# Optimization experiments

Hardware: AMD Instinct MI355X
Metric: run time of the kernel (lower is better)

Reference implementation:

```python
import jax, jax.numpy as jnp
import numpy as np

B, E, D, H, A = 65536, 16, 256, 64, 18  # batch, n_subpolicies, emb_dim, hidden, n_actions


def setup_inputs() -> dict:
    key = jax.random.key(0)
    ks = jax.random.split(key, 16)
    s = lambda k, sh: jax.random.normal(k, sh, dtype=jnp.float32) * 0.05
    return dict(
        obs=s(ks[0], (B, D)),
        h=s(ks[1], (B, D)),
        c=s(ks[2], (B, D)),
        idxs=jax.random.randint(ks[3], (B,), 0, E, dtype=jnp.int32),
        # Observer: LSTMCell(D, D) params (torch layout: [4D, D] with i,f,g,o gate order)
        W_ih=s(ks[4], (4 * D, D)), W_hh=s(ks[5], (4 * D, D)),
        b_ih=s(ks[6], (4 * D,)), b_hh=s(ks[7], (4 * D,)),
        # Stacked SubPolicy actor params: Linear(D,64)-Tanh-Linear(64,A)
        Wa1=s(ks[8], (E, D, H)), ba1=s(ks[9], (E, H)),
        Wa2=s(ks[10], (E, H, A)), ba2=s(ks[11], (E, A)),
        # Stacked SubPolicy critic params: Linear(D,64)-Tanh-Linear(64,1)
        Wc1=s(ks[12], (E, D, H)), bc1=s(ks[13], (E, H)),
        Wc2=s(ks[14], (E, H, 1)), bc2=s(ks[15], (E, 1)),
    )


def reference(obs, h, c, idxs, W_ih, W_hh, b_ih, b_hh,
              Wa1, ba1, Wa2, ba2, Wc1, bc1, Wc2, bc2):
    # ---- Observer: single LSTMCell step ----
    gates = obs @ W_ih.T + b_ih + h @ W_hh.T + b_hh          # [B, 4D]
    gi, gf, gg, go = jnp.split(gates, 4, axis=1)
    i = jax.nn.sigmoid(gi); f = jax.nn.sigmoid(gf); o = jax.nn.sigmoid(go)
    c_new = f * c + i * jnp.tanh(gg)                          # [B, D]
    h_new = o * jnp.tanh(c_new)                               # [B, D]

    # ---- Expert dispatch: evaluate all tiny subpolicy MLPs, select per sample ----
    # (mathematically identical to the per-sample routing loop in forward_sub)
    ha = jnp.tanh(jnp.einsum('bd,edh->beh', h_new, Wa1) + ba1)        # [B, E, H]
    logits_all = jnp.einsum('beh,eha->bea', ha, Wa2) + ba2            # [B, E, A]
    hc = jnp.tanh(jnp.einsum('bd,edh->beh', h_new, Wc1) + bc1)        # [B, E, H]
    vals_all = (jnp.einsum('beh,eho->beo', hc, Wc2) + bc2)[..., 0]    # [B, E]

    b = jnp.arange(h_new.shape[0])
    logits = logits_all[b, idxs]                                       # [B, A]
    values = vals_all[b, idxs]                                         # [B]
    return (h_new, c_new, logits, values)
```

## Files before the change

### kernel.cpp

```cpp
#include <hip/hip_runtime.h>
#include <hip/hip_bf16.h>
#include <math.h>

#define NB 65536
#define ND 256
#define NE 16
#define NH 64
#define NA 18

typedef __bf16 bf16;
typedef __bf16 bf16x4 __attribute__((ext_vector_type(4)));
typedef __bf16 bf16x8 __attribute__((ext_vector_type(8)));
typedef float  f32x4  __attribute__((ext_vector_type(4)));

#define OFF_WCAT 0u
#define OFF_BCAT 1048576u
#define OFF_PW1  1052672u
#define OFF_B1   2101248u
#define OFF_CUR  2109440u
#define OFF_PERM 2109504u

__device__ __forceinline__ float rcp_(float x) { return __builtin_amdgcn_rcpf(x); }
__device__ __forceinline__ float sigm_(float x) { return rcp_(1.f + __expf(-x)); }
__device__ __forceinline__ float tanh_(float x) {
    float cl = fminf(fmaxf(x, -15.f), 15.f);
    float e = __expf(2.f * cl);
    return (e - 1.f) * rcp_(e + 1.f);
}

__device__ __forceinline__ void gl2lds16(const void* g, void* l) {
    __builtin_amdgcn_global_load_lds(
        (const __attribute__((address_space(1))) unsigned int*)g,
        (__attribute__((address_space(3))) unsigned int*)l, 16, 0, 0);
}

__global__ void k_prep1(const float* __restrict__ W_ih, const float* __restrict__ W_hh,
                        const float* __restrict__ b_ih, const float* __restrict__ b_hh,
                        char* __restrict__ ws) {
    int t = blockIdx.x * 256 + threadIdx.x;
    int kstep = t >> 13;
    int cb    = (t >> 11) & 3;
    int idx   = t & 2047;
    int kf = idx >> 10, g = (idx >> 8) & 3, lk = (idx >> 6) & 3, u = idx & 63;
    int col = g * 256 + cb * 64 + (u ^ lk);
    int k0  = kstep * 64 + (kf * 4 + lk) * 8;
    const float* src = (k0 < 256) ? (W_ih + (size_t)col * 256 + k0)
                                  : (W_hh + (size_t)col * 256 + (k0 - 256));
    float4 v0 = *(const float4*)(src);
    float4 v1 = *(const float4*)(src + 4);
    bf16x8 o;
    o[0] = (bf16)v0.x; o[1] = (bf16)v0.y; o[2] = (bf16)v0.z; o[3] = (bf16)v0.w;
    o[4] = (bf16)v1.x; o[5] = (bf16)v1.y; o[6] = (bf16)v1.z; o[7] = (bf16)v1.w;
    *(bf16x8*)((bf16*)(ws + OFF_WCAT) + (size_t)t * 8) = o;
    if (t < 1024) ((float*)(ws + OFF_BCAT))[t] = b_ih[t] + b_hh[t];
    if (t < 16)   ((int*)(ws + OFF_CUR))[t] = t * 65536;
}

__global__ void k_prep2(const float* __restrict__ Wa1, const float* __restrict__ Wc1,
                        const float* __restrict__ ba1, const float* __restrict__ bc1,
                        char* __restrict__ ws) {
    int t = blockIdx.x * 256 + threadIdx.x;
    bf16* PW1 = (bf16*)(ws + OFF_PW1);
    int col = t & 127, kc = (t >> 7) & 31, e = t >> 12;
    bf16x8 o;
#pragma unroll
    for (int j = 0; j < 8; ++j) {
        int k = kc * 8 + j;
        float v = (col < 64) ? Wa1[((size_t)e * 256 + k) * 64 + col]
                             : Wc1[((size_t)e * 256 + k) * 64 + (col - 64)];
        o[j] = (bf16)v;
    }
    *(bf16x8*)(PW1 + (((size_t)e * 32 + kc) * 128 + col) * 8) = o;
    if (t < 2048) {
        int e2 = t >> 7, c = t & 127;
        ((float*)(ws + OFF_B1))[t] = (c < 64) ? ba1[e2 * 64 + c] : bc1[e2 * 64 + (c - 64)];
    }
}

__global__ void k_scatter(const int* __restrict__ idxs, char* __restrict__ ws) {
    __shared__ int lh[16], lbase[16];
    int t = threadIdx.x;
    int i = blockIdx.x * 256 + t;
    if (t < 16) lh[t] = 0;
    __syncthreads();
    int e = idxs[i];
    int r = atomicAdd(&lh[e], 1);
    __syncthreads();
    int* cur = (int*)(ws + OFF_CUR);
    if (t < 16) lbase[t] = atomicAdd(&cur[t], lh[t]);
    __syncthreads();
    ((int*)(ws + OFF_PERM))[lbase[e] + r] = i;
}

__global__ __launch_bounds__(256, 2) void k_lstm(
    const float* __restrict__ obs, const float* __restrict__ hin,
    const float* __restrict__ cin, const float* __restrict__ bcat,
    const char* __restrict__ wcat,
    float* __restrict__ hout, float* __restrict__ cout) {
    __shared__ alignas(16) char Abuf[2][8192];
    __shared__ alignas(16) char Bbuf[2][32768];
    const int tid  = threadIdx.x;
    const int w = tid >> 6, lane = tid & 63;
    const int lr = lane & 15, lk = lane >> 4;
    const int rb = blockIdx.x >> 2, cb = blockIdx.x & 3;
    const int row0 = rb * 64;
    const int colc = cb * 64 + w * 16 + lr;
    const int srw = tid >> 3, sj = tid & 7;

    const char* WcatBlk = wcat + (size_t)cb * 32768;
    const float* baseO0 = obs + (size_t)(row0 + srw) * 256 + sj * 8;
    const float* baseH0 = hin + (size_t)(row0 + srw) * 256 + sj * 8;

    int offE[4], offO[4];
#pragma unroll
    for (int m = 0; m < 4; ++m) {
        int R = m * 16 + lr;
        offE[m] = lk * 1024 + ((R ^ lk) * 16);
        offO[m] = (lk + 4) * 1024 + ((R ^ (lk + 4)) * 16);
    }
    const int bBase = lk * 1024 + (((w * 16 + lr) ^ lk) * 16);

    f32x4 acc[4][4];
#pragma unroll
    for (int m = 0; m < 4; ++m)
#pragma unroll
        for (int g = 0; g < 4; ++g)
#pragma unroll
            for (int r = 0; r < 4; ++r) acc[m][g][r] = 0.f;

#define STAGE_B(bi, ks)                                                      \
    {                                                                        \
        const char* srcB_ = WcatBlk + (size_t)(ks) * 131072;                 \
        _Pragma("unroll")                                                    \
        for (int i_ = 0; i_ < 8; ++i_) {                                     \
            int so_ = (w * 8 + i_) * 1024;                                   \
            gl2lds16(srcB_ + so_ + lane * 16, &Bbuf[bi][so_]);               \
        }                                                                    \
    }
#define LOAD_A(ks, d0, d1, d2, d3)                                           \
    {                                                                        \
        const float* s0_ = ((ks) < 4) ? (baseO0 + (ks) * 64)                 \
                                      : (baseH0 + ((ks) - 4) * 64);          \
        d0 = *(const float4*)(s0_);                                          \
        d1 = *(const float4*)(s0_ + 4);                                      \
        d2 = *(const float4*)(s0_ + 32 * 256);                               \
        d3 = *(const float4*)(s0_ + 32 * 256 + 4);                           \
    }
#define WRITE_A(bi, d0, d1, d2, d3)                                          \
    {                                                                        \
        bf16x8 oa_, ob_;                                                     \
        oa_[0] = (bf16)d0.x; oa_[1] = (bf16)d0.y; oa_[2] = (bf16)d0.z;       \
        oa_[3] = (bf16)d0.w; oa_[4] = (bf16)d1.x; oa_[5] = (bf16)d1.y;       \
        oa_[6] = (bf16)d1.z; oa_[7] = (bf16)d1.w;                            \
        ob_[0] = (bf16)d2.x; ob_[1] = (bf16)d2.y; ob_[2] = (bf16)d2.z;       \
        ob_[3] = (bf16)d2.w; ob_[4] = (bf16)d3.x; ob_[5] = (bf16)d3.y;       \
        ob_[6] = (bf16)d3.z; ob_[7] = (bf16)d3.w;                            \
        *(bf16x8*)(&Abuf[bi][sj * 1024 + ((srw ^ sj) * 16)]) = oa_;          \
        *(bf16x8*)(&Abuf[bi][sj * 1024 + (((srw + 32) ^ sj) * 16)]) = ob_;   \
    }
#define MFMA_STEP(cur)                                                       \
    {                                                                        \
        _Pragma("unroll")                                                    \
        for (int kf = 0; kf < 2; ++kf) {                                     \
            const char* Ab = Abuf[cur];                                      \
            const int* offA = kf ? offO : offE;                              \
            bf16x8 a0 = *(const bf16x8*)(Ab + offA[0]);                      \
            bf16x8 a1 = *(const bf16x8*)(Ab + offA[1]);                      \
            bf16x8 a2 = *(const bf16x8*)(Ab + offA[2]);                      \
            bf16x8 a3 = *(const bf16x8*)(Ab + offA[3]);                      \
            const char* Bb = Bbuf[cur] + kf * 16384 + bBase;                 \
            bf16x8 b0 = *(const bf16x8*)(Bb);                                \
            bf16x8 b1 = *(const bf16x8*)(Bb + 4096);                         \
            bf16x8 b2 = *(const bf16x8*)(Bb + 8192);                         \
            bf16x8 b3 = *(const bf16x8*)(Bb + 12288);                        \
            acc[0][0] = __builtin_amdgcn_mfma_f32_16x16x32_bf16(a0, b0, acc[0][0], 0, 0, 0); \
            acc[1][0] = __builtin_amdgcn_mfma_f32_16x16x32_bf16(a1, b0, acc[1][0], 0, 0, 0); \
            acc[2][0] = __builtin_amdgcn_mfma_f32_16x16x32_bf16(a2, b0, acc[2][0], 0, 0, 0); \
            acc[3][0] = __builtin_amdgcn_mfma_f32_16x16x32_bf16(a3, b0, acc[3][0], 0, 0, 0); \
            acc[0][1] = __builtin_amdgcn_mfma_f32_16x16x32_bf16(a0, b1, acc[0][1], 0, 0, 0); \
            acc[1][1] = __builtin_amdgcn_mfma_f32_16x16x32_bf16(a1, b1, acc[1][1], 0, 0, 0); \
            acc[2][1] = __builtin_amdgcn_mfma_f32_16x16x32_bf16(a2, b1, acc[2][1], 0, 0, 0); \
            acc[3][1] = __builtin_amdgcn_mfma_f32_16x16x32_bf16(a3, b1, acc[3][1], 0, 0, 0); \
            acc[0][2] = __builtin_amdgcn_mfma_f32_16x16x32_bf16(a0, b2, acc[0][2], 0, 0, 0); \
            acc[1][2] = __builtin_amdgcn_mfma_f32_16x16x32_bf16(a1, b2, acc[1][2], 0, 0, 0); \
            acc[2][2] = __builtin_amdgcn_mfma_f32_16x16x32_bf16(a2, b2, acc[2][2], 0, 0, 0); \
            acc[3][2] = __builtin_amdgcn_mfma_f32_16x16x32_bf16(a3, b2, acc[3][2], 0, 0, 0); \
            acc[0][3] = __builtin_amdgcn_mfma_f32_16x16x32_bf16(a0, b3, acc[0][3], 0, 0, 0); \
            acc[1][3] = __builtin_amdgcn_mfma_f32_16x16x32_bf16(a1, b3, acc[1][3], 0, 0, 0); \
            acc[2][3] = __builtin_amdgcn_mfma_f32_16x16x32_bf16(a2, b3, acc[2][3], 0, 0, 0); \
            acc[3][3] = __builtin_amdgcn_mfma_f32_16x16x32_bf16(a3, b3, acc[3][3], 0, 0, 0); \
        }                                                                    \
    }

    float4 pA0, pA1, pA2, pA3;
    float4 pB0, pB1, pB2, pB3;
    float cpre[16];

    LOAD_A(0, pA0, pA1, pA2, pA3);
    STAGE_B(0, 0);
    WRITE_A(0, pA0, pA1, pA2, pA3);
    LOAD_A(1, pA0, pA1, pA2, pA3);
    __syncthreads();

#pragma unroll
    for (int t = 0; t < 8; ++t) {
        const int cur = t & 1;
        if (t < 7) STAGE_B(cur ^ 1, t + 1);
        if ((t & 1) == 0) {
            if (t + 2 < 8) { LOAD_A(t + 2, pB0, pB1, pB2, pB3); }
        } else {
            if (t + 2 < 8) { LOAD_A(t + 2, pA0, pA1, pA2, pA3); }
        }
        if (t == 6) {
#pragma unroll
            for (int m = 0; m < 4; ++m)
#pragma unroll
                for (int r = 0; r < 4; ++r)
                    cpre[m * 4 + r] = cin[(size_t)(row0 + m * 16 + lk * 4 + r) * 256 + colc];
        }
        MFMA_STEP(cur);
        if (t < 7) {
            if ((t & 1) == 0) { WRITE_A(cur ^ 1, pA0, pA1, pA2, pA3); }
            else              { WRITE_A(cur ^ 1, pB0, pB1, pB2, pB3); }
            __syncthreads();
        }
    }
#undef STAGE_B
#undef LOAD_A
#undef WRITE_A
#undef MFMA_STEP

    float bi = bcat[colc], bf_ = bcat[256 + colc], bg = bcat[512 + colc], bo = bcat[768 + colc];
#pragma unroll
    for (int m = 0; m < 4; ++m) {
#pragma unroll
        for (int r = 0; r < 4; ++r) {
            int row = row0 + m * 16 + lk * 4 + r;
            float gi = acc[m][0][r] + bi;
            float gf = acc[m][1][r] + bf_;
            float gg = acc[m][2][r] + bg;
            float go = acc[m][3][r] + bo;
            float iv = sigm_(gi), fv = sigm_(gf), gv = tanh_(gg), ov = sigm_(go);
            float cn = fv * cpre[m * 4 + r] + iv * gv;
            float hn = ov * tanh_(cn);
            cout[(size_t)row * 256 + colc] = cn;
            hout[(size_t)row * 256 + colc] = hn;
        }
    }
}

__global__ __launch_bounds__(256) void k_expert(
    const float* __restrict__ Wa2, const float* __restrict__ ba2,
    const float* __restrict__ Wc2, const float* __restrict__ bc2,
    char* __restrict__ ws, const float* __restrict__ hsrc,
    float* __restrict__ lout, float* __restrict__ vout) {
    const int e = blockIdx.y;
    const int* cur = (const int*)(ws + OFF_CUR);
    int cnt = cur[e] - e * 65536;
    int r0 = blockIdx.x * 64;
    if (r0 >= cnt) return;
    int nr = min(64, cnt - r0);
    const int* permE = (const int*)(ws + OFF_PERM) + (size_t)e * 65536 + r0;

    __shared__ int rows_s[64];
    __shared__ alignas(16) char smem[128 * 66 * 4];
    bf16*  Alds = (bf16*)smem;
    float* haF  = (float*)smem;

    int t = threadIdx.x;
    if (t < 64) rows_s[t] = permE[(t < nr) ? t : 0];
    __syncthreads();

    {
        int rowi = t >> 2, q = t & 3;
        const float* hp = hsrc + (size_t)rows_s[rowi] * 256;
#pragma unroll
        for (int s = 0; s < 8; ++s) {
            int kc = s * 4 + q;
            float4 v0 = *(const float4*)(hp + kc * 8);
            float4 v1 = *(const float4*)(hp + kc * 8 + 4);
            bf16x8 o;
            o[0] = (bf16)v0.x; o[1] = (bf16)v0.y; o[2] = (bf16)v0.z; o[3] = (bf16)v0.w;
            o[4] = (bf16)v1.x; o[5] = (bf16)v1.y; o[6] = (bf16)v1.z; o[7] = (bf16)v1.w;
            *(bf16x8*)(Alds + ((size_t)kc * 64 + rowi) * 8) = o;
        }
    }
    __syncthreads();

    const bf16* PW1 = (const bf16*)(ws + OFF_PW1) + (size_t)e * 32 * 128 * 8;
    const float* b1 = (const float*)(ws + OFF_B1) + e * 128;
    int wave = t >> 6, lane = t & 63, lr = lane & 15, lk = lane >> 4;

    f32x4 acc[4][2];
#pragma unroll
    for (int m = 0; m < 4; ++m)
#pragma unroll
        for (int n = 0; n < 2; ++n)
#pragma unroll
            for (int r = 0; r < 4; ++r) acc[m][n][r] = 0.f;

#pragma unroll
    for (int kf = 0; kf < 8; ++kf) {
        bf16x8 a[4], bb[2];
#pragma unroll
        for (int m = 0; m < 4; ++m)
            a[m] = *(const bf16x8*)(Alds + (((kf * 4 + lk) * 64) + (m * 16 + lr)) * 8);
#pragma unroll
        for (int n = 0; n < 2; ++n) {
            int colh = wave * 32 + n * 16 + lr;
            int kc = kf * 4 + lk;
            bb[n] = *(const bf16x8*)(PW1 + ((size_t)kc * 128 + colh) * 8);
        }
#pragma unroll
        for (int m = 0; m < 4; ++m)
#pragma unroll
            for (int n = 0; n < 2; ++n)
                acc[m][n] = __builtin_amdgcn_mfma_f32_16x16x32_bf16(a[m], bb[n], acc[m][n], 0, 0, 0);
    }
    __syncthreads();

#pragma unroll
    for (int m = 0; m < 4; ++m)
#pragma unroll
        for (int n = 0; n < 2; ++n) {
            int colh = wave * 32 + n * 16 + lr;
            float bbv = b1[colh];
#pragma unroll
            for (int r = 0; r < 4; ++r) {
                int row = m * 16 + lk * 4 + r;
                haF[colh * 66 + row] = tanh_(acc[m][n][r] + bbv);
            }
        }
    __syncthreads();

    int row = t & 63;
    int grow = rows_s[row];
    bool valid = row < nr;
#pragma unroll
    for (int p = 0; p < 5; ++p) {
        int aI = p * 4 + (t >> 6);
        if (aI < NA) {
            float s = ba2[e * NA + aI];
            for (int hh = 0; hh < 64; ++hh)
                s += haF[hh * 66 + row] * Wa2[((size_t)e * 64 + hh) * NA + aI];
            if (valid) lout[(size_t)grow * NA + aI] = s;
        }
    }
    if (t < 64) {
        float s = bc2[e];
        for (int hh = 0; hh < 64; ++hh)
            s += haF[(64 + hh) * 66 + row] * Wc2[e * 64 + hh];
        if (valid) vout[grow] = s;
    }
}

extern "C" void kernel_launch(void* const* d_in, const int* in_sizes, int n_in,
                              void* d_out, int out_size, void* d_ws, size_t ws_size,
                              hipStream_t stream) {
    const float* obs  = (const float*)d_in[0];
    const float* h    = (const float*)d_in[1];
    const float* c    = (const float*)d_in[2];
    const int*   idxs = (const int*)d_in[3];
    const float* W_ih = (const float*)d_in[4];
    const float* W_hh = (const float*)d_in[5];
    const float* b_ih = (const float*)d_in[6];
    const float* b_hh = (const float*)d_in[7];
    const float* Wa1  = (const float*)d_in[8];
    const float* ba1  = (const float*)d_in[9];
    const float* Wa2  = (const float*)d_in[10];
    const float* ba2  = (const float*)d_in[11];
    const float* Wc1  = (const float*)d_in[12];
    const float* bc1  = (const float*)d_in[13];
    const float* Wc2  = (const float*)d_in[14];
    const float* bc2  = (const float*)d_in[15];

    float* out  = (float*)d_out;
    float* hout = out;
    float* cout = out + (size_t)NB * ND;
    float* lout = out + (size_t)2 * NB * ND;
    float* vout = lout + (size_t)NB * NA;
    char* ws = (char*)d_ws;

    k_prep1<<<dim3(256), dim3(256), 0, stream>>>(W_ih, W_hh, b_ih, b_hh, ws);
    k_prep2<<<dim3(256), dim3(256), 0, stream>>>(Wa1, Wc1, ba1, bc1, ws);
    k_scatter<<<dim3(256), dim3(256), 0, stream>>>(idxs, ws);
    k_lstm<<<dim3(4096), dim3(256), 0, stream>>>(
        obs, h, c, (const float*)(ws + OFF_BCAT), (const char*)(ws + OFF_WCAT), hout, cout);
    k_expert<<<dim3(1024, 16), dim3(256), 0, stream>>>(
        Wa2, ba2, Wc2, bc2, ws, hout, lout, vout);
}
```

Before: 217.3 us.

## Single-buffer LSTM weight tile in LDS, raise occupancy, remap blocks across XCDs

The LSTM GEMM kernel drops the double-buffered B tile in LDS and keeps one 32KB buffer. Each step first reads all B fragments into registers, syncs, then issues the next global-to-LDS copy while the MFMAs run from registers. This cuts LDS per block so the launch bound can rise from 2 to 3 blocks per CU, and it uses a single A prefetch register set. Block IDs are also remapped so blocks on the same XCD share column blocks and nearby rows, for better L2 reuse. The cost is an extra barrier per step and more register pressure from holding eight B fragments.

```diff
diff --git a/kernel.cpp b/kernel.cpp
--- a/kernel.cpp
+++ b/kernel.cpp
@@ -92,17 +92,20 @@
     ((int*)(ws + OFF_PERM))[lbase[e] + r] = i;
 }
 
-__global__ __launch_bounds__(256, 2) void k_lstm(
+__global__ __launch_bounds__(256, 3) void k_lstm(
     const float* __restrict__ obs, const float* __restrict__ hin,
     const float* __restrict__ cin, const float* __restrict__ bcat,
     const char* __restrict__ wcat,
     float* __restrict__ hout, float* __restrict__ cout) {
     __shared__ alignas(16) char Abuf[2][8192];
-    __shared__ alignas(16) char Bbuf[2][32768];
+    __shared__ alignas(16) char Bbuf[32768];
     const int tid  = threadIdx.x;
     const int w = tid >> 6, lane = tid & 63;
     const int lr = lane & 15, lk = lane >> 4;
-    const int rb = blockIdx.x >> 2, cb = blockIdx.x & 3;
+    const int bid = blockIdx.x;
+    const int xcd = bid & 7, rest = bid >> 3;
+    const int cb = rest & 3;
+    const int rb = ((rest >> 2) << 3) | xcd;
     const int row0 = rb * 64;
     const int colc = cb * 64 + w * 16 + lr;
     const int srw = tid >> 3, sj = tid & 7;
@@ -128,89 +131,83 @@
 #pragma unroll
             for (int r = 0; r < 4; ++r) acc[m][g][r] = 0.f;
 
-#define STAGE_B(bi, ks)                                                      \
+#define STAGE_B(ks)                                                          \
     {                                                                        \
         const char* srcB_ = WcatBlk + (size_t)(ks) * 131072;                 \
         _Pragma("unroll")                                                    \
         for (int i_ = 0; i_ < 8; ++i_) {                                     \
             int so_ = (w * 8 + i_) * 1024;                                   \
-            gl2lds16(srcB_ + so_ + lane * 16, &Bbuf[bi][so_]);               \
+            gl2lds16(srcB_ + so_ + lane * 16, &Bbuf[so_]);                   \
         }                                                                    \
     }
-#define LOAD_A(ks, d0, d1, d2, d3)                                           \
+#define LOAD_A(ks)                                                           \
     {                                                                        \
         const float* s0_ = ((ks) < 4) ? (baseO0 + (ks) * 64)                 \
                                       : (baseH0 + ((ks) - 4) * 64);          \
-        d0 = *(const float4*)(s0_);                                          \
-        d1 = *(const float4*)(s0_ + 4);                                      \
-        d2 = *(const float4*)(s0_ + 32 * 256);                               \
-        d3 = *(const float4*)(s0_ + 32 * 256 + 4);                           \
-    }
-#define WRITE_A(bi, d0, d1, d2, d3)                                          \
+        pf0 = *(const float4*)(s0_);                                         \
+        pf1 = *(const float4*)(s0_ + 4);                                     \
+        pf2 = *(const float4*)(s0_ + 32 * 256);                              \
+        pf3 = *(const float4*)(s0_ + 32 * 256 + 4);                          \
+    }
+#define WRITE_A(bi)                                                          \
     {                                                                        \
         bf16x8 oa_, ob_;                                                     \
-        oa_[0] = (bf16)d0.x; oa_[1] = (bf16)d0.y; oa_[2] = (bf16)d0.z;       \
-        oa_[3] = (bf16)d0.w; oa_[4] = (bf16)d1.x; oa_[5] = (bf16)d1.y;       \
-        oa_[6] = (bf16)d1.z; oa_[7] = (bf16)d1.w;                            \
-        ob_[0] = (bf16)d2.x; ob_[1] = (bf16)d2.y; ob_[2] = (bf16)d2.z;       \
-        ob_[3] = (bf16)d2.w; ob_[4] = (bf16)d3.x; ob_[5] = (bf16)d3.y;       \
-        ob_[6] = (bf16)d3.z; ob_[7] = (bf16)d3.w;                            \
+        oa_[0] = (bf16)pf0.x; oa_[1] = (bf16)pf0.y; oa_[2] = (bf16)pf0.z;    \
+        oa_[3] = (bf16)pf0.w; oa_[4] = (bf16)pf1.x; oa_[5] = (bf16)pf1.y;    \
+        oa_[6] = (bf16)pf1.z; oa_[7] = (bf16)pf1.w;                          \
+        ob_[0] = (bf16)pf2.x; ob_[1] = (bf16)pf2.y; ob_[2] = (bf16)pf2.z;    \
+        ob_[3] = (bf16)pf2.w; ob_[4] = (bf16)pf3.x; ob_[5] = (bf16)pf3.y;    \
+        ob_[6] = (bf16)pf3.z; ob_[7] = (bf16)pf3.w;                          \
         *(bf16x8*)(&Abuf[bi][sj * 1024 + ((srw ^ sj) * 16)]) = oa_;          \
         *(bf16x8*)(&Abuf[bi][sj * 1024 + (((srw + 32) ^ sj) * 16)]) = ob_;   \
     }
-#define MFMA_STEP(cur)                                                       \
+#define MFMA_HALF(cur, offA, q0, q1, q2, q3)                                 \
     {                                                                        \
-        _Pragma("unroll")                                                    \
-        for (int kf = 0; kf < 2; ++kf) {                                     \
-            const char* Ab = Abuf[cur];                                      \
-            const int* offA = kf ? offO : offE;                              \
-            bf16x8 a0 = *(const bf16x8*)(Ab + offA[0]);                      \
-            bf16x8 a1 = *(const bf16x8*)(Ab + offA[1]);                      \
-            bf16x8 a2 = *(const bf16x8*)(Ab + offA[2]);                      \
-            bf16x8 a3 = *(const bf16x8*)(Ab + offA[3]);                      \
-            const char* Bb = Bbuf[cur] + kf * 16384 + bBase;                 \
-            bf16x8 b0 = *(const bf16x8*)(Bb);                                \
-            bf16x8 b1 = *(const bf16x8*)(Bb + 4096);                         \
-            bf16x8 b2 = *(const bf16x8*)(Bb + 8192);                         \
-            bf16x8 b3 = *(const bf16x8*)(Bb + 12288);                        \
-            acc[0][0] = __builtin_amdgcn_mfma_f32_16x16x32_bf16(a0, b0, acc[0][0], 0, 0, 0); \
-            acc[1][0] = __builtin_amdgcn_mfma_f32_16x16x32_bf16(a1, b0, acc[1][0], 0, 0, 0); \
-            acc[2][0] = __builtin_amdgcn_mfma_f32_16x16x32_bf16(a2, b0, acc[2][0], 0, 0, 0); \
-            acc[3][0] = __builtin_amdgcn_mfma_f32_16x16x32_bf16(a3, b0, acc[3][0], 0, 0, 0); \
-            acc[0][1] = __builtin_amdgcn_mfma_f32_16x16x32_bf16(a0, b1, acc[0][1], 0, 0, 0); \
-            acc[1][1] = __builtin_amdgcn_mfma_f32_16x16x32_bf16(a1, b1, acc[1][1], 0, 0, 0); \
-            acc[2][1] = __builtin_amdgcn_mfma_f32_16x16x32_bf16(a2, b1, acc[2][1], 0, 0, 0); \
-            acc[3][1] = __builtin_amdgcn_mfma_f32_16x16x32_bf16(a3, b1, acc[3][1], 0, 0, 0); \
-            acc[0][2] = __builtin_amdgcn_mfma_f32_16x16x32_bf16(a0, b2, acc[0][2], 0, 0, 0); \
-            acc[1][2] = __builtin_amdgcn_mfma_f32_16x16x32_bf16(a1, b2, acc[1][2], 0, 0, 0); \
-            acc[2][2] = __builtin_amdgcn_mfma_f32_16x16x32_bf16(a2, b2, acc[2][2], 0, 0, 0); \
-            acc[3][2] = __builtin_amdgcn_mfma_f32_16x16x32_bf16(a3, b2, acc[3][2], 0, 0, 0); \
-            acc[0][3] = __builtin_amdgcn_mfma_f32_16x16x32_bf16(a0, b3, acc[0][3], 0, 0, 0); \
-            acc[1][3] = __builtin_amdgcn_mfma_f32_16x16x32_bf16(a1, b3, acc[1][3], 0, 0, 0); \
-            acc[2][3] = __builtin_amdgcn_mfma_f32_16x16x32_bf16(a2, b3, acc[2][3], 0, 0, 0); \
-            acc[3][3] = __builtin_amdgcn_mfma_f32_16x16x32_bf16(a3, b3, acc[3][3], 0, 0, 0); \
-        }                                                                    \
-    }
-
-    float4 pA0, pA1, pA2, pA3;
-    float4 pB0, pB1, pB2, pB3;
+        const char* Ab_ = Abuf[cur];                                         \
+        bf16x8 a0 = *(const bf16x8*)(Ab_ + offA[0]);                         \
+        bf16x8 a1 = *(const bf16x8*)(Ab_ + offA[1]);                         \
+        bf16x8 a2 = *(const bf16x8*)(Ab_ + offA[2]);                         \
+        bf16x8 a3 = *(const bf16x8*)(Ab_ + offA[3]);                         \
+        acc[0][0] = __builtin_amdgcn_mfma_f32_16x16x32_bf16(a0, q0, acc[0][0], 0, 0, 0); \
+        acc[1][0] = __builtin_amdgcn_mfma_f32_16x16x32_bf16(a1, q0, acc[1][0], 0, 0, 0); \
+        acc[2][0] = __builtin_amdgcn_mfma_f32_16x16x32_bf16(a2, q0, acc[2][0], 0, 0, 0); \
+        acc[3][0] = __builtin_amdgcn_mfma_f32_16x16x32_bf16(a3, q0, acc[3][0], 0, 0, 0); \
+        acc[0][1] = __builtin_amdgcn_mfma_f32_16x16x32_bf16(a0, q1, acc[0][1], 0, 0, 0); \
+        acc[1][1] = __builtin_amdgcn_mfma_f32_16x16x32_bf16(a1, q1, acc[1][1], 0, 0, 0); \
+        acc[2][1] = __builtin_amdgcn_mfma_f32_16x16x32_bf16(a2, q1, acc[2][1], 0, 0, 0); \
+        acc[3][1] = __builtin_amdgcn_mfma_f32_16x16x32_bf16(a3, q1, acc[3][1], 0, 0, 0); \
+        acc[0][2] = __builtin_amdgcn_mfma_f32_16x16x32_bf16(a0, q2, acc[0][2], 0, 0, 0); \
+        acc[1][2] = __builtin_amdgcn_mfma_f32_16x16x32_bf16(a1, q2, acc[1][2], 0, 0, 0); \
+        acc[2][2] = __builtin_amdgcn_mfma_f32_16x16x32_bf16(a2, q2, acc[2][2], 0, 0, 0); \
+        acc[3][2] = __builtin_amdgcn_mfma_f32_16x16x32_bf16(a3, q2, acc[3][2], 0, 0, 0); \
+        acc[0][3] = __builtin_amdgcn_mfma_f32_16x16x32_bf16(a0, q3, acc[0][3], 0, 0, 0); \
+        acc[1][3] = __builtin_amdgcn_mfma_f32_16x16x32_bf16(a1, q3, acc[1][3], 0, 0, 0); \
+        acc[2][3] = __builtin_amdgcn_mfma_f32_16x16x32_bf16(a2, q3, acc[2][3], 0, 0, 0); \
+        acc[3][3] = __builtin_amdgcn_mfma_f32_16x16x32_bf16(a3, q3, acc[3][3], 0, 0, 0); \
+    }
+
+    float4 pf0, pf1, pf2, pf3;
     float cpre[16];
 
-    LOAD_A(0, pA0, pA1, pA2, pA3);
-    STAGE_B(0, 0);
-    WRITE_A(0, pA0, pA1, pA2, pA3);
-    LOAD_A(1, pA0, pA1, pA2, pA3);
+    LOAD_A(0);
+    STAGE_B(0);
+    WRITE_A(0);
+    LOAD_A(1);
     __syncthreads();
 
 #pragma unroll
     for (int t = 0; t < 8; ++t) {
         const int cur = t & 1;
-        if (t < 7) STAGE_B(cur ^ 1, t + 1);
-        if ((t & 1) == 0) {
-            if (t + 2 < 8) { LOAD_A(t + 2, pB0, pB1, pB2, pB3); }
-        } else {
-            if (t + 2 < 8) { LOAD_A(t + 2, pA0, pA1, pA2, pA3); }
-        }
+        const char* Bb0 = Bbuf + bBase;
+        bf16x8 br0 = *(const bf16x8*)(Bb0);
+        bf16x8 br1 = *(const bf16x8*)(Bb0 + 4096);
+        bf16x8 br2 = *(const bf16x8*)(Bb0 + 8192);
+        bf16x8 br3 = *(const bf16x8*)(Bb0 + 12288);
+        bf16x8 br4 = *(const bf16x8*)(Bb0 + 16384);
+        bf16x8 br5 = *(const bf16x8*)(Bb0 + 20480);
+        bf16x8 br6 = *(const bf16x8*)(Bb0 + 24576);
+        bf16x8 br7 = *(const bf16x8*)(Bb0 + 28672);
+        __syncthreads();
         if (t == 6) {
 #pragma unroll
             for (int m = 0; m < 4; ++m)
@@ -218,17 +215,19 @@
                 for (int r = 0; r < 4; ++r)
                     cpre[m * 4 + r] = cin[(size_t)(row0 + m * 16 + lk * 4 + r) * 256 + colc];
         }
-        MFMA_STEP(cur);
         if (t < 7) {
-            if ((t & 1) == 0) { WRITE_A(cur ^ 1, pA0, pA1, pA2, pA3); }
-            else              { WRITE_A(cur ^ 1, pB0, pB1, pB2, pB3); }
-            __syncthreads();
-        }
+            STAGE_B(t + 1);
+            WRITE_A(cur ^ 1);
+        }
+        if (t < 6) LOAD_A(t + 2);
+        MFMA_HALF(cur, offE, br0, br1, br2, br3);
+        MFMA_HALF(cur, offO, br4, br5, br6, br7);
+        if (t < 7) __syncthreads();
     }
 #undef STAGE_B
 #undef LOAD_A
 #undef WRITE_A
-#undef MFMA_STEP
+#undef MFMA_HALF
 
     float bi = bcat[colc], bf_ = bcat[256 + colc], bg = bcat[512 + colc], bo = bcat[768 + colc];
 #pragma unroll
```

After: 199.9 us. 8.0% less time.

## Hand-schedule LSTM GEMM pipeline with explicit waitcnts and XCD-aware block mapping

Applied to the files above, without the earlier changes.

Replaces the loop-based double-buffered LSTM GEMM with an explicitly unrolled pipeline. Each step issues the next A prefetch and B stage first, waits on vmcnt with tuned counts, raises wave priority around the MFMA block, and uses raw s_barrier instead of __syncthreads. It also remaps block IDs so that the four column blocks sharing a row tile land on the same XCD, to improve L2 reuse of the obs/h rows. The hand-tuned vmcnt values are fragile: if the load counts don't match, the kernel risks reading data before it has arrived.

```diff
diff --git a/kernel.cpp b/kernel.cpp
--- a/kernel.cpp
+++ b/kernel.cpp
@@ -102,7 +102,10 @@
     const int tid  = threadIdx.x;
     const int w = tid >> 6, lane = tid & 63;
     const int lr = lane & 15, lk = lane >> 4;
-    const int rb = blockIdx.x >> 2, cb = blockIdx.x & 3;
+    const int bid = blockIdx.x;
+    const int xcd = bid & 7, rest = bid >> 3;
+    const int cb = rest & 3;
+    const int rb = ((rest >> 2) << 3) | xcd;
     const int row0 = rb * 64;
     const int colc = cb * 64 + w * 16 + lr;
     const int srw = tid >> 3, sj = tid & 7;
@@ -191,44 +194,55 @@
             acc[3][3] = __builtin_amdgcn_mfma_f32_16x16x32_bf16(a3, b3, acc[3][3], 0, 0, 0); \
         }                                                                    \
     }
-
-    float4 pA0, pA1, pA2, pA3;
-    float4 pB0, pB1, pB2, pB3;
+#define PIPE_STEP(T, CUR, LD0, LD1, LD2, LD3, WR0, WR1, WR2, WR3, KN)        \
+    {                                                                        \
+        if ((T) + 2 < 8) LOAD_A((T) + 2, LD0, LD1, LD2, LD3);                \
+        if ((T) + 1 < 8) STAGE_B((CUR) ^ 1, (T) + 1);                        \
+        if ((T) == 6) {                                                      \
+            _Pragma("unroll")                                                \
+            for (int m = 0; m < 4; ++m)                                      \
+                _Pragma("unroll")                                            \
+                for (int r = 0; r < 4; ++r)                                  \
+                    cpre[m * 4 + r] =                                        \
+                        cin[(size_t)(row0 + m * 16 + lk * 4 + r) * 256 + colc]; \
+        }                                                                    \
+        asm volatile("s_waitcnt vmcnt(" #KN ")" ::: "memory");               \
+        __builtin_amdgcn_sched_barrier(0);                                   \
+        __builtin_amdgcn_s_setprio(1);                                       \
+        MFMA_STEP(CUR);                                                      \
+        __builtin_amdgcn_s_setprio(0);                                       \
+        if ((T) + 1 < 8) {                                                   \
+            WRITE_A((CUR) ^ 1, WR0, WR1, WR2, WR3);                          \
+            asm volatile("s_waitcnt lgkmcnt(0)" ::: "memory");               \
+            __builtin_amdgcn_s_barrier();                                    \
+        }                                                                    \
+    }
+
+    float4 a0_, a1_, a2_, a3_;
+    float4 b0_, b1_, b2_, b3_;
     float cpre[16];
 
-    LOAD_A(0, pA0, pA1, pA2, pA3);
+    LOAD_A(0, a0_, a1_, a2_, a3_);
     STAGE_B(0, 0);
-    WRITE_A(0, pA0, pA1, pA2, pA3);
-    LOAD_A(1, pA0, pA1, pA2, pA3);
-    __syncthreads();
-
-#pragma unroll
-    for (int t = 0; t < 8; ++t) {
-        const int cur = t & 1;
-        if (t < 7) STAGE_B(cur ^ 1, t + 1);
-        if ((t & 1) == 0) {
-            if (t + 2 < 8) { LOAD_A(t + 2, pB0, pB1, pB2, pB3); }
-        } else {
-            if (t + 2 < 8) { LOAD_A(t + 2, pA0, pA1, pA2, pA3); }
-        }
-        if (t == 6) {
-#pragma unroll
-            for (int m = 0; m < 4; ++m)
-#pragma unroll
-                for (int r = 0; r < 4; ++r)
-                    cpre[m * 4 + r] = cin[(size_t)(row0 + m * 16 + lk * 4 + r) * 256 + colc];
-        }
-        MFMA_STEP(cur);
-        if (t < 7) {
-            if ((t & 1) == 0) { WRITE_A(cur ^ 1, pA0, pA1, pA2, pA3); }
-            else              { WRITE_A(cur ^ 1, pB0, pB1, pB2, pB3); }
-            __syncthreads();
-        }
-    }
+    WRITE_A(0, a0_, a1_, a2_, a3_);
+    LOAD_A(1, a0_, a1_, a2_, a3_);
+    asm volatile("s_waitcnt lgkmcnt(0)" ::: "memory");
+    __builtin_amdgcn_s_barrier();
+
+    PIPE_STEP(0, 0, b0_, b1_, b2_, b3_, a0_, a1_, a2_, a3_, 12);
+    PIPE_STEP(1, 1, a0_, a1_, a2_, a3_, b0_, b1_, b2_, b3_, 12);
+    PIPE_STEP(2, 0, b0_, b1_, b2_, b3_, a0_, a1_, a2_, a3_, 12);
+    PIPE_STEP(3, 1, a0_, a1_, a2_, a3_, b0_, b1_, b2_, b3_, 12);
+    PIPE_STEP(4, 0, b0_, b1_, b2_, b3_, a0_, a1_, a2_, a3_, 12);
+    PIPE_STEP(5, 1, a0_, a1_, a2_, a3_, b0_, b1_, b2_, b3_, 12);
+    PIPE_STEP(6, 0, b0_, b1_, b2_, b3_, a0_, a1_, a2_, a3_, 24);
+    PIPE_STEP(7, 1, a0_, a1_, a2_, a3_, b0_, b1_, b2_, b3_, 16);
+
 #undef STAGE_B
 #undef LOAD_A
 #undef WRITE_A
 #undef MFMA_STEP
+#undef PIPE_STEP
 
     float bi = bcat[colc], bf_ = bcat[256 + colc], bg = bcat[512 + colc], bo = bcat[768 + colc];
 #pragma unroll
```

Measured after the change: 205.6 us. -5.4%, faster.
